# Performance work log

Measured on AMD Instinct MI355X. Metric: run time of the kernel, lower is better.

Reference implementation:

```python
import jax, jax.numpy as jnp
import numpy as np

N = 50000        # nodes
E = 600000       # edges
D = 128          # hidden dim
FID = 128        # fixed_input_dim (one-hot size)
RWSE = 16        # rwse_dim
G = 128          # num graphs
L = 4            # num GIN blocks
DEG = 1001       # degree embedding table (clamp to 1000)
GIN_EPS = 0.0
BN_EPS = 1e-5


def setup_inputs() -> dict:
    key = jax.random.key(0)
    ks = jax.random.split(key, 16)
    s = 0.05
    inp = {
        "feat_id": jax.random.randint(ks[0], (N,), 0, 100000),
        "edge_index": jax.random.randint(ks[1], (2, E), 0, N),
        "batch_idx": jnp.sort(jax.random.randint(ks[2], (N,), 0, G)),
        "rwse": jax.random.normal(ks[3], (N, RWSE), jnp.float32),
        "in_degrees": jax.random.randint(ks[4], (N,), 0, DEG),
        # parameters
        "value_W": jax.random.normal(ks[5], (FID, D), jnp.float32) * s,
        "value_b": jnp.zeros((D,), jnp.float32),
        "rwse_W": jax.random.normal(ks[6], (RWSE, D), jnp.float32) * s,
        "rwse_b": jnp.zeros((D,), jnp.float32),
        "deg_emb": jax.random.normal(ks[7], (DEG, D), jnp.float32) * s,
        "mlp_W1": jax.random.normal(ks[8], (L, D, D), jnp.float32) * s,
        "mlp_b1": jnp.zeros((L, D), jnp.float32),
        "mlp_W2": jax.random.normal(ks[9], (L, D, D), jnp.float32) * s,
        "mlp_b2": jnp.zeros((L, D), jnp.float32),
        "bn_gamma": 1.0 + jax.random.normal(ks[10], (L, D), jnp.float32) * s,
        "bn_beta": jax.random.normal(ks[11], (L, D), jnp.float32) * s,
        "bn_mean": jax.random.normal(ks[12], (L, D), jnp.float32) * s,
        "bn_var": 1.0 + jax.random.uniform(ks[13], (L, D), jnp.float32) * 0.1,
    }
    return inp


def reference(feat_id, edge_index, batch_idx, rwse, in_degrees,
              value_W, value_b, rwse_W, rwse_b, deg_emb,
              mlp_W1, mlp_b1, mlp_W2, mlp_b2,
              bn_gamma, bn_beta, bn_mean, bn_var):
    # one_hot(feat_id % FID) @ value_W  ==  row gather of value_W
    h_id = jnp.remainder(feat_id, FID)
    h_attr = value_W[h_id] + value_b                      # [N, D]
    h_attr = h_attr + rwse @ rwse_W + rwse_b              # rwse projection
    deg = jnp.clip(in_degrees, 0, DEG - 1)
    h = h_attr + deg_emb[deg]                             # [N, D]

    src, dst = edge_index[0], edge_index[1]
    for l in range(L):
        # GIN aggregation: sum of neighbor messages + (1+eps)*self
        agg = jax.ops.segment_sum(h[src], dst, num_segments=N)
        agg = agg + (1.0 + GIN_EPS) * h
        # MLP: Linear -> ReLU -> Linear
        m = jax.nn.relu(agg @ mlp_W1[l] + mlp_b1[l]) @ mlp_W2[l] + mlp_b2[l]
        # BatchNorm (inference stats) + ReLU
        inv = bn_gamma[l] * jax.lax.rsqrt(bn_var[l] + BN_EPS)
        h = jax.nn.relu((m - bn_mean[l]) * inv + bn_beta[l])

    # scatter-mean graph pooling
    pooled = jax.ops.segment_sum(h, batch_idx, num_segments=G)      # [G, D]
    count = jax.ops.segment_sum(jnp.ones((N, 1), h.dtype), batch_idx,
                                num_segments=G)                     # [G, 1]
    graph_feature = pooled / jnp.maximum(count, 1.0)
    return graph_feature, h
```

## Files before the change

kernel.cpp:

```cpp
#include <hip/hip_runtime.h>

#define N_NODES 50000
#define N_EDGES 600000
#define DIM 128
#define NGRAPH 128
#define NLAYER 4
#define BN_EPS 1e-5f
#define SCAN_BLK 1024

#define EN_BLOCKS 3125
#define WT_BLOCKS 512
#define HB_BLOCKS 2344

using short8  = __attribute__((ext_vector_type(8))) short;
using float4v = __attribute__((ext_vector_type(4))) float;

__device__ __forceinline__ float bf2f(unsigned short u) {
    union { unsigned int i; float f; } c; c.i = ((unsigned int)u) << 16; return c.f;
}
__device__ __forceinline__ unsigned short f2bf(float f) {
    union { float f; unsigned int i; } c; c.f = f;
    unsigned int x = c.i;
    return (unsigned short)((x + 0x7fffu + ((x >> 16) & 1u)) >> 16);
}

__global__ void fused_pre_kernel(const int* __restrict__ feat_id,
                                 const float* __restrict__ rwse,
                                 const int* __restrict__ indeg,
                                 const float* __restrict__ value_W,
                                 const float* __restrict__ value_b,
                                 const float* __restrict__ rwse_W,
                                 const float* __restrict__ rwse_b,
                                 const float* __restrict__ deg_emb,
                                 unsigned short* __restrict__ hout,
                                 const float* __restrict__ W1,
                                 const float* __restrict__ W2,
                                 unsigned short* __restrict__ w1t,
                                 unsigned short* __restrict__ w2t,
                                 const int* __restrict__ dst,
                                 int* __restrict__ cnt)
{
    int b = blockIdx.x;
    if (b < EN_BLOCKS) {
        __shared__ float srw[16][16];
        __shared__ int   sfid[16], sdeg[16];
        const int t = threadIdx.x;
        const int base = b * 16;
        srw[t >> 4][t & 15] = rwse[(size_t)base * 16 + t];
        if (t < 16) sfid[t] = feat_id[base + t] & 127;
        else if (t < 32) {
            int dg = indeg[base + t - 16];
            sdeg[t - 16] = dg < 0 ? 0 : (dg > 1000 ? 1000 : dg);
        }
        const int d = t & 127, half = t >> 7;
        float wk[16];
#pragma unroll
        for (int k = 0; k < 16; ++k) wk[k] = rwse_W[k * DIM + d];
        float vb = value_b[d] + rwse_b[d];
        __syncthreads();
#pragma unroll
        for (int nn = 0; nn < 8; ++nn) {
            int nl = half * 8 + nn;
            int node = base + nl;
            float v = value_W[sfid[nl] * DIM + d] + vb + deg_emb[sdeg[nl] * DIM + d];
            float acc = 0.f;
#pragma unroll
            for (int k = 0; k < 16; ++k) acc += srw[nl][k] * wk[k];
            hout[(size_t)node * DIM + d] = f2bf(v + acc);
        }
    } else if (b < EN_BLOCKS + WT_BLOCKS) {
        int idx = (b - EN_BLOCKS) * 256 + threadIdx.x;
        int i = idx & (DIM * DIM - 1);
        int l = (idx >> 14) & 3;
        int is2 = idx >= NLAYER * DIM * DIM;
        int n = i >> 7, k = i & 127;
        const float* W = (is2 ? W2 : W1) + l * DIM * DIM;
        unsigned short v = f2bf(W[k * DIM + n]);
        (is2 ? w2t : w1t)[l * DIM * DIM + n * DIM + k] = v;
    } else {
        int e = (b - EN_BLOCKS - WT_BLOCKS) * 256 + threadIdx.x;
        if (e < N_EDGES) atomicAdd(&cnt[dst[e]], 1);
    }
}

__global__ void scanA_kernel(const int* __restrict__ cnt, int* __restrict__ rp, int* __restrict__ bsum) {
    __shared__ int sc[SCAN_BLK];
    int t = threadIdx.x, i = blockIdx.x * SCAN_BLK + t;
    int v = (i < N_NODES) ? cnt[i] : 0;
    sc[t] = v; __syncthreads();
    for (int off = 1; off < SCAN_BLK; off <<= 1) {
        int add = (t >= off) ? sc[t - off] : 0;
        __syncthreads();
        sc[t] += add;
        __syncthreads();
    }
    if (i < N_NODES) rp[i] = sc[t] - v;
    if (t == SCAN_BLK - 1) bsum[blockIdx.x] = sc[t];
}

__global__ void scan_fixup_kernel(int* __restrict__ rp, const int* __restrict__ bsum,
                                  int* __restrict__ cur, int nsb) {
    __shared__ int sbx[64];
    int t = threadIdx.x;
    if (t < 64) {
        int v = (t < nsb) ? bsum[t] : 0;
        int orig = v;
        for (int off = 1; off < 64; off <<= 1) {
            int y = __shfl_up(v, off, 64);
            if (t >= off) v += y;
        }
        sbx[t] = v - orig;
    }
    __syncthreads();
    int i = blockIdx.x * 256 + t;
    if (i < N_NODES) { int v = rp[i] + sbx[i >> 10]; rp[i] = v; cur[i] = v; }
    else if (i == N_NODES) rp[i] = N_EDGES;
}

__global__ void scatter_kernel(const int* __restrict__ src, const int* __restrict__ dst,
                               int* __restrict__ cur, int* __restrict__ esrc) {
    int e = blockIdx.x * blockDim.x + threadIdx.x;
    if (e < N_EDGES) {
        int pos = atomicAdd(&cur[dst[e]], 1);
        esrc[pos] = src[e];
    }
}

__global__ void __launch_bounds__(256, 8) layer_kernel(
    const unsigned short* __restrict__ hin,
    const int* __restrict__ rp,
    const int* __restrict__ esrc,
    const unsigned short* __restrict__ w1t,
    const unsigned short* __restrict__ w2t,
    const float* __restrict__ b1, const float* __restrict__ b2,
    const float* __restrict__ gam, const float* __restrict__ bet,
    const float* __restrict__ mean, const float* __restrict__ var,
    unsigned short* __restrict__ hout, float* __restrict__ fout, int last)
{
    __shared__ unsigned short sA[16 * DIM];
    __shared__ unsigned short sM[16 * DIM];
    const int tid = threadIdx.x;
    const int wave = tid >> 6, lane = tid & 63;
    const int fr = lane & 15, fg = lane >> 4;
    const int base = blockIdx.x * 16;

    for (int j = 0; j < 4; ++j) {
        int row = wave * 4 + j;
        int node = __builtin_amdgcn_readfirstlane(base + row);
        float a[8];
#pragma unroll
        for (int i = 0; i < 8; ++i) a[i] = 0.f;
        if (fg == 0) {
            uint4 s = *(const uint4*)(hin + (size_t)node * DIM + fr * 8);
            a[0] = bf2f((unsigned short)(s.x & 0xffff)); a[1] = bf2f((unsigned short)(s.x >> 16));
            a[2] = bf2f((unsigned short)(s.y & 0xffff)); a[3] = bf2f((unsigned short)(s.y >> 16));
            a[4] = bf2f((unsigned short)(s.z & 0xffff)); a[5] = bf2f((unsigned short)(s.z >> 16));
            a[6] = bf2f((unsigned short)(s.w & 0xffff)); a[7] = bf2f((unsigned short)(s.w >> 16));
        }
        int e1 = rp[node + 1];
        int e = rp[node] + fg;
        int snext = (e < e1) ? esrc[e] : 0;
        while (e < e1) {
            int s = snext;
            int en = e + 4;
            snext = (en < e1) ? esrc[en] : 0;
            uint4 v = *(const uint4*)(hin + (size_t)s * DIM + fr * 8);
            a[0] += bf2f((unsigned short)(v.x & 0xffff)); a[1] += bf2f((unsigned short)(v.x >> 16));
            a[2] += bf2f((unsigned short)(v.y & 0xffff)); a[3] += bf2f((unsigned short)(v.y >> 16));
            a[4] += bf2f((unsigned short)(v.z & 0xffff)); a[5] += bf2f((unsigned short)(v.z >> 16));
            a[6] += bf2f((unsigned short)(v.w & 0xffff)); a[7] += bf2f((unsigned short)(v.w >> 16));
            e = en;
        }
#pragma unroll
        for (int i = 0; i < 8; ++i) {
            a[i] += __shfl_xor(a[i], 16, 64);
            a[i] += __shfl_xor(a[i], 32, 64);
        }
        if (fg == 0) {
            uint4 o;
            o.x = (unsigned int)f2bf(a[0]) | ((unsigned int)f2bf(a[1]) << 16);
            o.y = (unsigned int)f2bf(a[2]) | ((unsigned int)f2bf(a[3]) << 16);
            o.z = (unsigned int)f2bf(a[4]) | ((unsigned int)f2bf(a[5]) << 16);
            o.w = (unsigned int)f2bf(a[6]) | ((unsigned int)f2bf(a[7]) << 16);
            int byte = row * 256 + fr * 16; byte ^= (row & 7) << 4;
            *(uint4*)((char*)sA + byte) = o;
        }
    }
    __syncthreads();

    short8 a0, a1, a2, a3;
    {
        int sw = (fr & 7) << 4;
        a0 = *(const short8*)((char*)sA + ((fr * 256 + (0  + fg * 8) * 2) ^ sw));
        a1 = *(const short8*)((char*)sA + ((fr * 256 + (32 + fg * 8) * 2) ^ sw));
        a2 = *(const short8*)((char*)sA + ((fr * 256 + (64 + fg * 8) * 2) ^ sw));
        a3 = *(const short8*)((char*)sA + ((fr * 256 + (96 + fg * 8) * 2) ^ sw));
    }

    float4v acc[2];
    acc[0] = (float4v){0.f, 0.f, 0.f, 0.f};
    acc[1] = (float4v){0.f, 0.f, 0.f, 0.f};

    const unsigned short* bp1 = w1t + (wave * 32 + fr) * DIM + fg * 8;
#pragma unroll
    for (int nb = 0; nb < 2; ++nb) {
        const unsigned short* bb = bp1 + nb * 16 * DIM;
        short8 b0 = *(const short8*)(bb);
        short8 b1v = *(const short8*)(bb + 32);
        short8 b2v = *(const short8*)(bb + 64);
        short8 b3v = *(const short8*)(bb + 96);
        acc[nb] = __builtin_amdgcn_mfma_f32_16x16x32_bf16(a0, b0, acc[nb], 0, 0, 0);
        acc[nb] = __builtin_amdgcn_mfma_f32_16x16x32_bf16(a1, b1v, acc[nb], 0, 0, 0);
        acc[nb] = __builtin_amdgcn_mfma_f32_16x16x32_bf16(a2, b2v, acc[nb], 0, 0, 0);
        acc[nb] = __builtin_amdgcn_mfma_f32_16x16x32_bf16(a3, b3v, acc[nb], 0, 0, 0);
    }

#pragma unroll
    for (int nb = 0; nb < 2; ++nb) {
        int col = wave * 32 + nb * 16 + fr;
        float bias = b1[col];
#pragma unroll
        for (int r = 0; r < 4; ++r) {
            int row = fg * 4 + r;
            float v = acc[nb][r] + bias;
            v = fmaxf(v, 0.f);
            int byte = row * 256 + col * 2; byte ^= (row & 7) << 4;
            *(unsigned short*)((char*)sM + byte) = f2bf(v);
        }
    }
    __syncthreads();

    short8 m0, m1, m2, m3;
    {
        int sw = (fr & 7) << 4;
        m0 = *(const short8*)((char*)sM + ((fr * 256 + (0  + fg * 8) * 2) ^ sw));
        m1 = *(const short8*)((char*)sM + ((fr * 256 + (32 + fg * 8) * 2) ^ sw));
        m2 = *(const short8*)((char*)sM + ((fr * 256 + (64 + fg * 8) * 2) ^ sw));
        m3 = *(const short8*)((char*)sM + ((fr * 256 + (96 + fg * 8) * 2) ^ sw));
    }

    float4v acc2[2];
    acc2[0] = (float4v){0.f, 0.f, 0.f, 0.f};
    acc2[1] = (float4v){0.f, 0.f, 0.f, 0.f};

    const unsigned short* bp2 = w2t + (wave * 32 + fr) * DIM + fg * 8;
#pragma unroll
    for (int nb = 0; nb < 2; ++nb) {
        const unsigned short* bb = bp2 + nb * 16 * DIM;
        short8 b0 = *(const short8*)(bb);
        short8 b1v = *(const short8*)(bb + 32);
        short8 b2v = *(const short8*)(bb + 64);
        short8 b3v = *(const short8*)(bb + 96);
        acc2[nb] = __builtin_amdgcn_mfma_f32_16x16x32_bf16(m0, b0, acc2[nb], 0, 0, 0);
        acc2[nb] = __builtin_amdgcn_mfma_f32_16x16x32_bf16(m1, b1v, acc2[nb], 0, 0, 0);
        acc2[nb] = __builtin_amdgcn_mfma_f32_16x16x32_bf16(m2, b2v, acc2[nb], 0, 0, 0);
        acc2[nb] = __builtin_amdgcn_mfma_f32_16x16x32_bf16(m3, b3v, acc2[nb], 0, 0, 0);
    }

#pragma unroll
    for (int nb = 0; nb < 2; ++nb) {
        int col = wave * 32 + nb * 16 + fr;
        float bias = b2[col];
        float iv = gam[col] * rsqrtf(var[col] + BN_EPS);
        float mn = mean[col], bt = bet[col];
#pragma unroll
        for (int r = 0; r < 4; ++r) {
            int node = base + fg * 4 + r;
            float v = acc2[nb][r] + bias;
            v = (v - mn) * iv + bt;
            v = fmaxf(v, 0.f);
            if (last) fout[(size_t)node * DIM + col] = v;
            else hout[(size_t)node * DIM + col] = f2bf(v);
        }
    }
}

__global__ void __launch_bounds__(256) pool_partial_kernel(const float* __restrict__ h,
                                                           const int* __restrict__ batch,
                                                           float* __restrict__ partial)
{
    __shared__ float sums[256];
    __shared__ int sb[2];
    int g = blockIdx.x >> 3, split = blockIdx.x & 7;
    if (threadIdx.x < 2) {
        int target = g + threadIdx.x;
        int lo = 0, hi = N_NODES;
        while (lo < hi) { int mid = (lo + hi) >> 1; if (batch[mid] < target) lo = mid + 1; else hi = mid; }
        sb[threadIdx.x] = lo;
    }
    __syncthreads();
    int lo = sb[0], hi = sb[1];
    int d = threadIdx.x & 127, half = threadIdx.x >> 7;
    float acc = 0.f;
    for (int n = lo + split * 2 + half; n < hi; n += 16) acc += h[(size_t)n * DIM + d];
    sums[threadIdx.x] = acc;
    __syncthreads();
    if (threadIdx.x < 128)
        partial[blockIdx.x * DIM + threadIdx.x] = sums[threadIdx.x] + sums[threadIdx.x + 128];
}

__global__ void pool_comb_kernel(const float* __restrict__ partial,
                                 const int* __restrict__ batch,
                                 float* __restrict__ out)
{
    __shared__ int sb[2];
    int g = blockIdx.x, t = threadIdx.x;
    if (t < 2) {
        int target = g + t;
        int lo = 0, hi = N_NODES;
        while (lo < hi) { int mid = (lo + hi) >> 1; if (batch[mid] < target) lo = mid + 1; else hi = mid; }
        sb[t] = lo;
    }
    __syncthreads();
    float s = 0.f;
#pragma unroll
    for (int sp = 0; sp < 8; ++sp) s += partial[(g * 8 + sp) * DIM + t];
    float c = (float)(sb[1] - sb[0]);
    out[g * DIM + t] = s / fmaxf(c, 1.f);
}

extern "C" void kernel_launch(void* const* d_in, const int* in_sizes, int n_in,
                              void* d_out, int out_size, void* d_ws, size_t ws_size,
                              hipStream_t stream)
{
    const int*   feat_id = (const int*)d_in[0];
    const int*   eidx    = (const int*)d_in[1];
    const int*   batch   = (const int*)d_in[2];
    const float* rwse    = (const float*)d_in[3];
    const int*   indeg   = (const int*)d_in[4];
    const float* value_W = (const float*)d_in[5];
    const float* value_b = (const float*)d_in[6];
    const float* rwse_W  = (const float*)d_in[7];
    const float* rwse_b  = (const float*)d_in[8];
    const float* deg_emb = (const float*)d_in[9];
    const float* W1      = (const float*)d_in[10];
    const float* b1      = (const float*)d_in[11];
    const float* W2      = (const float*)d_in[12];
    const float* b2      = (const float*)d_in[13];
    const float* gam     = (const float*)d_in[14];
    const float* bet     = (const float*)d_in[15];
    const float* mean    = (const float*)d_in[16];
    const float* var     = (const float*)d_in[17];

    const int* srcv = eidx;
    const int* dstv = eidx + N_EDGES;

    char* p = (char*)d_ws;
    auto alloc = [&](size_t bytes) { char* r = p; p += (bytes + 255) & ~(size_t)255; return r; };
    unsigned short* hA   = (unsigned short*)alloc((size_t)N_NODES * DIM * 2);
    unsigned short* hB   = (unsigned short*)alloc((size_t)N_NODES * DIM * 2);
    int* cnt  = (int*)alloc((size_t)N_NODES * 4);
    int* rp   = (int*)alloc((size_t)(N_NODES + 1) * 4);
    int* cur  = (int*)alloc((size_t)N_NODES * 4);
    int* bsum = (int*)alloc(64 * 4);
    int* esrc = (int*)alloc((size_t)N_EDGES * 4);
    unsigned short* w1t = (unsigned short*)alloc((size_t)NLAYER * DIM * DIM * 2);
    unsigned short* w2t = (unsigned short*)alloc((size_t)NLAYER * DIM * DIM * 2);
    float* partial = (float*)alloc((size_t)NGRAPH * 8 * DIM * 4);

    float* out = (float*)d_out;
    float* hf  = out + NGRAPH * DIM;

    hipMemsetAsync(cnt, 0, (size_t)N_NODES * 4, stream);
    fused_pre_kernel<<<EN_BLOCKS + WT_BLOCKS + HB_BLOCKS, 256, 0, stream>>>(
        feat_id, rwse, indeg, value_W, value_b, rwse_W, rwse_b, deg_emb, hA,
        W1, W2, w1t, w2t, dstv, cnt);
    int nsb = (N_NODES + SCAN_BLK - 1) / SCAN_BLK;
    scanA_kernel<<<nsb, SCAN_BLK, 0, stream>>>(cnt, rp, bsum);
    scan_fixup_kernel<<<(N_NODES + 1 + 255) / 256, 256, 0, stream>>>(rp, bsum, cur, nsb);
    scatter_kernel<<<(N_EDGES + 255) / 256, 256, 0, stream>>>(srcv, dstv, cur, esrc);

    const int nlb = N_NODES / 16;
    for (int l = 0; l < NLAYER; ++l) {
        const unsigned short* hi = (l & 1) ? hB : hA;
        unsigned short*       ho = (l & 1) ? hA : hB;
        layer_kernel<<<nlb, 256, 0, stream>>>(hi, rp, esrc,
            w1t + l * DIM * DIM, w2t + l * DIM * DIM,
            b1 + l * DIM, b2 + l * DIM, gam + l * DIM, bet + l * DIM,
            mean + l * DIM, var + l * DIM,
            ho, hf, (l == NLAYER - 1) ? 1 : 0);
    }
    pool_partial_kernel<<<NGRAPH * 8, 256, 0, stream>>>(hf, batch, partial);
    pool_comb_kernel<<<NGRAPH, DIM, 0, stream>>>(partial, batch, out);
}
```

Baseline: 399.8 us.

## Stage neighbor rows in LDS via block-wide cooperative edge gather

```diff
diff --git a/kernel.cpp b/kernel.cpp
--- a/kernel.cpp
+++ b/kernel.cpp
@@ -22,6 +22,12 @@
     union { float f; unsigned int i; } c; c.f = f;
     unsigned int x = c.i;
     return (unsigned short)((x + 0x7fffu + ((x >> 16) & 1u)) >> 16);
+}
+__device__ __forceinline__ void acc8(float* a, uint4 v) {
+    a[0] += bf2f((unsigned short)(v.x & 0xffff)); a[1] += bf2f((unsigned short)(v.x >> 16));
+    a[2] += bf2f((unsigned short)(v.y & 0xffff)); a[3] += bf2f((unsigned short)(v.y >> 16));
+    a[4] += bf2f((unsigned short)(v.z & 0xffff)); a[5] += bf2f((unsigned short)(v.z >> 16));
+    a[6] += bf2f((unsigned short)(v.w & 0xffff)); a[7] += bf2f((unsigned short)(v.w >> 16));
 }
 
 __global__ void fused_pre_kernel(const int* __restrict__ feat_id,
@@ -126,7 +132,7 @@
     }
 }
 
-__global__ void __launch_bounds__(256, 8) layer_kernel(
+__global__ void __launch_bounds__(256, 6) layer_kernel(
     const unsigned short* __restrict__ hin,
     const int* __restrict__ rp,
     const int* __restrict__ esrc,
@@ -137,54 +143,76 @@
     const float* __restrict__ mean, const float* __restrict__ var,
     unsigned short* __restrict__ hout, float* __restrict__ fout, int last)
 {
+    __shared__ unsigned short sHg[64 * DIM];
     __shared__ unsigned short sA[16 * DIM];
     __shared__ unsigned short sM[16 * DIM];
+    __shared__ int sIdx[64];
+    __shared__ int sRp[17];
     const int tid = threadIdx.x;
     const int wave = tid >> 6, lane = tid & 63;
     const int fr = lane & 15, fg = lane >> 4;
+    const int grp = tid >> 4;
+    const int q = tid & 15;
     const int base = blockIdx.x * 16;
 
-    for (int j = 0; j < 4; ++j) {
-        int row = wave * 4 + j;
-        int node = __builtin_amdgcn_readfirstlane(base + row);
-        float a[8];
-#pragma unroll
-        for (int i = 0; i < 8; ++i) a[i] = 0.f;
-        if (fg == 0) {
-            uint4 s = *(const uint4*)(hin + (size_t)node * DIM + fr * 8);
-            a[0] = bf2f((unsigned short)(s.x & 0xffff)); a[1] = bf2f((unsigned short)(s.x >> 16));
-            a[2] = bf2f((unsigned short)(s.y & 0xffff)); a[3] = bf2f((unsigned short)(s.y >> 16));
-            a[4] = bf2f((unsigned short)(s.z & 0xffff)); a[5] = bf2f((unsigned short)(s.z >> 16));
-            a[6] = bf2f((unsigned short)(s.w & 0xffff)); a[7] = bf2f((unsigned short)(s.w >> 16));
-        }
-        int e1 = rp[node + 1];
-        int e = rp[node] + fg;
-        int snext = (e < e1) ? esrc[e] : 0;
-        while (e < e1) {
-            int s = snext;
-            int en = e + 4;
-            snext = (en < e1) ? esrc[en] : 0;
-            uint4 v = *(const uint4*)(hin + (size_t)s * DIM + fr * 8);
-            a[0] += bf2f((unsigned short)(v.x & 0xffff)); a[1] += bf2f((unsigned short)(v.x >> 16));
-            a[2] += bf2f((unsigned short)(v.y & 0xffff)); a[3] += bf2f((unsigned short)(v.y >> 16));
-            a[4] += bf2f((unsigned short)(v.z & 0xffff)); a[5] += bf2f((unsigned short)(v.z >> 16));
-            a[6] += bf2f((unsigned short)(v.w & 0xffff)); a[7] += bf2f((unsigned short)(v.w >> 16));
-            e = en;
-        }
-#pragma unroll
-        for (int i = 0; i < 8; ++i) {
-            a[i] += __shfl_xor(a[i], 16, 64);
-            a[i] += __shfl_xor(a[i], 32, 64);
-        }
-        if (fg == 0) {
-            uint4 o;
-            o.x = (unsigned int)f2bf(a[0]) | ((unsigned int)f2bf(a[1]) << 16);
-            o.y = (unsigned int)f2bf(a[2]) | ((unsigned int)f2bf(a[3]) << 16);
-            o.z = (unsigned int)f2bf(a[4]) | ((unsigned int)f2bf(a[5]) << 16);
-            o.w = (unsigned int)f2bf(a[6]) | ((unsigned int)f2bf(a[7]) << 16);
-            int byte = row * 256 + fr * 16; byte ^= (row & 7) << 4;
-            *(uint4*)((char*)sA + byte) = o;
-        }
+    if (tid < 17) sRp[tid] = rp[base + tid];
+
+    uint4 selfv = *(const uint4*)(hin + (size_t)(base + grp) * DIM + q * 8);
+    float a[8];
+#pragma unroll
+    for (int i = 0; i < 8; ++i) a[i] = 0.f;
+    acc8(a, selfv);
+
+    __syncthreads();
+    const int segS = sRp[0], segE = sRp[16];
+    const int myS = sRp[grp], myE = sRp[grp + 1];
+
+    if (tid < 64) sIdx[tid] = (segS + tid < segE) ? esrc[segS + tid] : 0;
+    __syncthreads();
+
+    for (int cb = segS; cb < segE; cb += 64) {
+        const int cnt = (segE - cb < 64) ? (segE - cb) : 64;
+        const int sl0 = grp, sl1 = grp + 16, sl2 = grp + 32, sl3 = grp + 48;
+        int i0 = sIdx[sl0], i1 = sIdx[sl1], i2 = sIdx[sl2], i3 = sIdx[sl3];
+        uint4 z = (uint4){0u, 0u, 0u, 0u};
+        uint4 v0 = (sl0 < cnt) ? *(const uint4*)(hin + (size_t)i0 * DIM + q * 8) : z;
+        uint4 v1 = (sl1 < cnt) ? *(const uint4*)(hin + (size_t)i1 * DIM + q * 8) : z;
+        uint4 v2 = (sl2 < cnt) ? *(const uint4*)(hin + (size_t)i2 * DIM + q * 8) : z;
+        uint4 v3 = (sl3 < cnt) ? *(const uint4*)(hin + (size_t)i3 * DIM + q * 8) : z;
+        {
+            int b0 = sl0 * 256 + q * 16; b0 ^= (sl0 & 7) << 4;
+            int b1b = sl1 * 256 + q * 16; b1b ^= (sl1 & 7) << 4;
+            int b2b = sl2 * 256 + q * 16; b2b ^= (sl2 & 7) << 4;
+            int b3b = sl3 * 256 + q * 16; b3b ^= (sl3 & 7) << 4;
+            *(uint4*)((char*)sHg + b0) = v0;
+            *(uint4*)((char*)sHg + b1b) = v1;
+            *(uint4*)((char*)sHg + b2b) = v2;
+            *(uint4*)((char*)sHg + b3b) = v3;
+        }
+        __syncthreads();
+
+        int nb2 = cb + 64;
+        if (nb2 < segE && tid < 64) sIdx[tid] = (nb2 + tid < segE) ? esrc[nb2 + tid] : 0;
+
+        int lo = (myS > cb) ? myS : cb;
+        int hi = (myE < cb + cnt) ? myE : (cb + cnt);
+        for (int t = lo; t < hi; ++t) {
+            int slot = t - cb;
+            int byte = slot * 256 + q * 16; byte ^= (slot & 7) << 4;
+            uint4 v = *(const uint4*)((char*)sHg + byte);
+            acc8(a, v);
+        }
+        __syncthreads();
+    }
+
+    {
+        uint4 o;
+        o.x = (unsigned int)f2bf(a[0]) | ((unsigned int)f2bf(a[1]) << 16);
+        o.y = (unsigned int)f2bf(a[2]) | ((unsigned int)f2bf(a[3]) << 16);
+        o.z = (unsigned int)f2bf(a[4]) | ((unsigned int)f2bf(a[5]) << 16);
+        o.w = (unsigned int)f2bf(a[6]) | ((unsigned int)f2bf(a[7]) << 16);
+        int byte = grp * 256 + q * 16; byte ^= (grp & 7) << 4;
+        *(uint4*)((char*)sA + byte) = o;
     }
     __syncthreads();
 
```

Result: faster. 390.6 us (-2.3%).
